# Optimization experiments

Measured on AMD Instinct MI355X. Metric: run time of the kernel, lower is better.

## Reference

```python
import jax, jax.numpy as jnp
import numpy as np

B, C, H, W = 16, 256, 96, 96
PLANES = 64            # inplanes * ratio = 256 * 0.25
HEADS = 4
EPS = 1e-5             # BatchNorm eps


def setup_inputs() -> dict:
    key = jax.random.key(0)
    ks = jax.random.split(key, 8)
    HW = H * W
    G = HW // HEADS    # group size of the grouped 1x1 conv over spatial-positions-as-channels
    return {
        "x": jax.random.normal(ks[0], (B, C, H, W), jnp.float32),
        # input_conv: Conv1x1(C->PLANES) -> BN -> ReLU -> Conv1x1(PLANES->C)
        "w1": jax.random.normal(ks[1], (PLANES, C), jnp.float32) * (1.0 / np.sqrt(C)),
        "b1": jax.random.normal(ks[2], (PLANES,), jnp.float32) * 0.01,
        "gamma": jnp.ones((PLANES,), jnp.float32),
        "beta": jnp.zeros((PLANES,), jnp.float32),
        "mean": jnp.zeros((PLANES,), jnp.float32),
        "var": jnp.ones((PLANES,), jnp.float32),
        "w2": jax.random.normal(ks[3], (C, PLANES), jnp.float32) * (1.0 / np.sqrt(PLANES)),
        "b2": jax.random.normal(ks[4], (C,), jnp.float32) * 0.01,
        # conv_mask: Conv2d(HW, HEADS, k=1, groups=HEADS) -> weight [HEADS, G], bias [HEADS]
        "wm": jax.random.normal(ks[5], (HEADS, G), jnp.float32) * (1.0 / np.sqrt(G)),
        "bm": jax.random.normal(ks[6], (HEADS,), jnp.float32) * 0.01,
    }


def reference(x, w1, b1, gamma, beta, mean, var, w2, b2, wm, bm):
    Bx, Cx, Hx, Wx = x.shape
    G = (Hx * Wx) // HEADS
    # ---- input_conv: 1x1 conv -> BN (inference) -> ReLU -> 1x1 conv ----
    h = jnp.einsum('bchw,pc->bphw', x, w1) + b1[None, :, None, None]
    scale = (gamma / jnp.sqrt(var + EPS))[None, :, None, None]
    h = jax.nn.relu((h - mean[None, :, None, None]) * scale + beta[None, :, None, None])
    y = jnp.einsum('bphw,cp->bchw', h, w2) + b2[None, :, None, None]
    # ---- treat spatial positions as channels: [B, HEADS, G, C] ----
    ix = y.transpose(0, 2, 3, 1).reshape(Bx, HEADS, G, Cx)
    # grouped 1x1 conv over HW-channels -> logits [B, HEADS, C]
    logits = jnp.einsum('bhgc,hg->bhc', ix, wm) + bm[None, :, None]
    # softmax over channel axis (torch dim=2 of [B, HEADS, C, 1])
    mask = jax.nn.softmax(logits, axis=2)
    # context pooling matmul: [B,HEADS,G,C] @ [B,HEADS,C,1] -> [B,HEADS,G]
    ctx = jnp.einsum('bhgc,bhc->bhg', ix, mask)
    context = ctx.reshape(Bx, 1, Hx, Wx)
    # fusion_types = ('channel_add',)
    return x + context
```

## Files before the change

kernel.cpp:

```cpp
#include <hip/hip_runtime.h>

#define Bn 16
#define Cn 256
#define HWn 9216
#define Pn 64
#define HEADSn 4
#define Gn 2304
#define STILE 64
#define TILES_PER_B (HWn / STILE)
#define NTILE (Bn * TILES_PER_B)
#define CHUNK 9
#define NBLK (NTILE / CHUNK)

typedef float f32x4 __attribute__((ext_vector_type(4)));
typedef short short4v __attribute__((ext_vector_type(4)));
typedef short short8 __attribute__((ext_vector_type(8)));

static __device__ __forceinline__ unsigned short f2bf(float f) {
    unsigned int b = __builtin_bit_cast(unsigned int, f);
    unsigned int r = b + 0x7FFFu + ((b >> 16) & 1u);
    return (unsigned short)(r >> 16);
}
static __device__ __forceinline__ float bf2f(unsigned short u) {
    unsigned int b = ((unsigned int)u) << 16;
    return __builtin_bit_cast(float, b);
}
static __device__ __forceinline__ void gload_lds16(const void* g, void* l) {
    __builtin_amdgcn_global_load_lds((const __attribute__((address_space(1))) void*)g,
                                     (__attribute__((address_space(3))) void*)l, 16, 0, 0);
}

__global__ __launch_bounds__(256)
void k0_prep(const float* __restrict__ w1, const float* __restrict__ b1,
             const float* __restrict__ gamma, const float* __restrict__ beta,
             const float* __restrict__ mean, const float* __restrict__ var,
             float* __restrict__ scbc, short* __restrict__ w1s)
{
    const int gid = blockIdx.x * 256 + threadIdx.x;
    if (gid < 2048) {
        const int row = gid >> 5;
        const int kc  = (gid & 31) << 3;
        const float* p = w1 + row * Cn + kc;
        short8 v;
        #pragma unroll
        for (int j = 0; j < 8; ++j) v[j] = (short)f2bf(p[j]);
        const int idx = (row * Cn + kc) ^ ((row & 7) << 3);
        *reinterpret_cast<short8*>(&w1s[idx]) = v;
    }
    if (gid < Pn) {
        float s = gamma[gid] * rsqrtf(var[gid] + 1e-5f);
        scbc[gid] = s;
        scbc[Pn + gid] = (b1[gid] - mean[gid]) * s + beta[gid];
    }
}

__global__ __launch_bounds__(256)
void k1_gemm(const float* __restrict__ x, const short* __restrict__ w1s,
             const float* __restrict__ scbc, const float* __restrict__ wm,
             float* __restrict__ hmp, short* __restrict__ hg)
{
    __shared__ short w1l[Pn * Cn];
    __shared__ short xl[2][Cn * STILE];
    __shared__ float hml[4][Pn];

    const int pid  = blockIdx.x;
    const int b    = pid / 16;
    const int t0b  = pid * CHUNK - b * TILES_PER_B;
    const int t    = threadIdx.x;
    const int lane = t & 63;
    const int wv   = t >> 6;
    const int g    = lane >> 4;
    const int m16  = lane & 15;
    const int sbase = wv * 16 + m16;

    #pragma unroll
    for (int i = 0; i < 8; ++i) {
        const int chunk = i * 4 + wv;
        gload_lds16(w1s + chunk * 512 + lane * 8, &w1l[chunk * 512]);
    }

    const int c0 = t >> 4;
    const int s4 = t & 15;
    const float* xbb = x + (size_t)b * Cn * HWn + s4 * 4;
    short* hgb = hg + (size_t)b * HWn * Pn;
    const float* scp = scbc;

    float sc[4][4], bc[4][4];
    #pragma unroll
    for (int rt = 0; rt < 4; ++rt)
        #pragma unroll
        for (int r = 0; r < 4; ++r) {
            const int p = rt * 16 + g * 4 + r;
            sc[rt][r] = scp[p];
            bc[rt][r] = scp[Pn + p];
        }

    float hmacc[4][4];
    #pragma unroll
    for (int rt = 0; rt < 4; ++rt)
        #pragma unroll
        for (int r = 0; r < 4; ++r) hmacc[rt][r] = 0.f;

    {
        const float* xb = xbb + (size_t)(t0b * STILE);
        f32x4 xa[16];
        #pragma unroll
        for (int i = 0; i < 16; ++i)
            xa[i] = *reinterpret_cast<const f32x4*>(xb + (size_t)(c0 + 16 * i) * HWn);
        #pragma unroll
        for (int i = 0; i < 16; ++i) {
            const int c = c0 + 16 * i;
            short4v v;
            #pragma unroll
            for (int j = 0; j < 4; ++j) v[j] = (short)f2bf(xa[i][j]);
            const int f   = (c & 7) ^ ((c >> 3) & 3);
            const int idx = (c * STILE + s4 * 4) ^ (f << 3);
            *reinterpret_cast<short4v*>(&xl[0][idx]) = v;
        }
    }
    __syncthreads();

    int cur = 0;
    for (int it = 0; it < CHUNK; ++it) {
        const int s0 = (t0b + it) * STILE;

        f32x4 xn[16];
        if (it < CHUNK - 1) {
            const float* xb = xbb + (size_t)(s0 + STILE);
            #pragma unroll
            for (int i = 0; i < 16; ++i)
                xn[i] = *reinterpret_cast<const f32x4*>(xb + (size_t)(c0 + 16 * i) * HWn);
        }

        const short* xc = xl[cur];
        f32x4 acc[4] = { {0,0,0,0}, {0,0,0,0}, {0,0,0,0}, {0,0,0,0} };
        #pragma unroll
        for (int ks = 0; ks < 8; ++ks) {
            short8 bf;
            #pragma unroll
            for (int j = 0; j < 8; ++j) {
                const int k = ks * 32 + g * 8 + j;
                bf[j] = xc[(k * STILE + sbase) ^ ((j ^ g) << 3)];
            }
            #pragma unroll
            for (int rt = 0; rt < 4; ++rt) {
                const int row = rt * 16 + m16;
                const int idx = (row * Cn + ks * 32 + g * 8) ^ ((row & 7) << 3);
                const short8 af = *reinterpret_cast<const short8*>(&w1l[idx]);
                acc[rt] = __builtin_amdgcn_mfma_f32_16x16x32_bf16(af, bf, acc[rt], 0, 0, 0);
            }
        }

        const float wmv = wm[s0 + sbase];
        short* hrow = hgb + (size_t)(s0 + sbase) * Pn;
        #pragma unroll
        for (int rt = 0; rt < 4; ++rt) {
            short4v hv;
            #pragma unroll
            for (int r = 0; r < 4; ++r) {
                float h = acc[rt][r] * sc[rt][r] + bc[rt][r];
                h = h > 0.f ? h : 0.f;
                hmacc[rt][r] = fmaf(h, wmv, hmacc[rt][r]);
                hv[r] = (short)f2bf(h);
            }
            *reinterpret_cast<short4v*>(hrow + rt * 16 + g * 4) = hv;
        }

        if (it < CHUNK - 1) {
            #pragma unroll
            for (int i = 0; i < 16; ++i) {
                const int c = c0 + 16 * i;
                short4v v;
                #pragma unroll
                for (int j = 0; j < 4; ++j) v[j] = (short)f2bf(xn[i][j]);
                const int f   = (c & 7) ^ ((c >> 3) & 3);
                const int idx = (c * STILE + s4 * 4) ^ (f << 3);
                *reinterpret_cast<short4v*>(&xl[cur ^ 1][idx]) = v;
            }
            __syncthreads();
            cur ^= 1;
        }
    }

    #pragma unroll
    for (int rt = 0; rt < 4; ++rt)
        #pragma unroll
        for (int r = 0; r < 4; ++r) {
            float v = hmacc[rt][r];
            v += __shfl_xor(v, 1); v += __shfl_xor(v, 2);
            v += __shfl_xor(v, 4); v += __shfl_xor(v, 8);
            hmacc[rt][r] = v;
        }
    if (m16 == 0) {
        #pragma unroll
        for (int rt = 0; rt < 4; ++rt) {
            f32x4 hv = { hmacc[rt][0], hmacc[rt][1], hmacc[rt][2], hmacc[rt][3] };
            *reinterpret_cast<f32x4*>(&hml[wv][rt * 16 + g * 4]) = hv;
        }
    }
    __syncthreads();
    if (t < Pn) hmp[pid * Pn + t] = hml[0][t] + hml[1][t] + hml[2][t] + hml[3][t];
}

__global__ __launch_bounds__(256)
void k2_mask(const float* __restrict__ hmp, const float* __restrict__ w2,
             const float* __restrict__ b2, const float* __restrict__ wm,
             float* __restrict__ wmix, float* __restrict__ bmix)
{
    __shared__ float hms[Pn];
    __shared__ float masks[Cn];
    __shared__ float red[4];
    __shared__ float part[4][Pn];

    const int bh = blockIdx.x;
    const int head = bh & (HEADSn - 1);
    const int t = threadIdx.x;
    const int l = t & 63;
    const int wv = t >> 6;

    {
        const int p = t & 63, q = t >> 6;
        part[q][p] = hmp[(bh * 4 + q) * Pn + p];
    }
    __syncthreads();
    if (t < Pn) hms[t] = part[0][t] + part[1][t] + part[2][t] + part[3][t];
    __syncthreads();

    float wsum = 0.f;
    for (int i = t; i < Gn; i += 256) wsum += wm[head * Gn + i];
    #pragma unroll
    for (int d = 1; d < 64; d <<= 1) wsum += __shfl_xor(wsum, d);
    if (l == 0) red[wv] = wsum;
    __syncthreads();
    wsum = red[0] + red[1] + red[2] + red[3];

    float lg = 0.f;
    #pragma unroll
    for (int k = 0; k < Pn; ++k) lg = fmaf(w2[t * Pn + k], hms[k], lg);
    lg = fmaf(b2[t], wsum, lg);

    float mx = lg;
    #pragma unroll
    for (int d = 1; d < 64; d <<= 1) mx = fmaxf(mx, __shfl_xor(mx, d));
    __syncthreads();
    if (l == 0) red[wv] = mx;
    __syncthreads();
    mx = fmaxf(fmaxf(red[0], red[1]), fmaxf(red[2], red[3]));
    const float ev = __expf(lg - mx);
    float sm = ev;
    #pragma unroll
    for (int d = 1; d < 64; d <<= 1) sm += __shfl_xor(sm, d);
    __syncthreads();
    if (l == 0) red[wv] = sm;
    __syncthreads();
    sm = red[0] + red[1] + red[2] + red[3];
    masks[t] = ev / sm;
    __syncthreads();

    {
        const int k = t & (Pn - 1);
        const int q = t >> 6;
        float wp = 0.f;
        #pragma unroll
        for (int i = 0; i < 64; ++i) {
            const int c = q * 64 + i;
            wp = fmaf(masks[c], w2[c * Pn + k], wp);
        }
        part[q][k] = wp;
    }
    __syncthreads();
    if (t < Pn) wmix[bh * Pn + t] = part[0][t] + part[1][t] + part[2][t] + part[3][t];

    float bp = masks[t] * b2[t];
    #pragma unroll
    for (int d = 1; d < 64; d <<= 1) bp += __shfl_xor(bp, d);
    __syncthreads();
    if (l == 0) red[wv] = bp;
    __syncthreads();
    if (t == 0) bmix[bh] = red[0] + red[1] + red[2] + red[3];
}

__global__ __launch_bounds__(256)
void k3_stream(const float* __restrict__ x, const short* __restrict__ hg,
               const float* __restrict__ wmix, const float* __restrict__ bmix,
               float* __restrict__ out)
{
    __shared__ float ctxl[STILE];

    const int bid  = blockIdx.x;
    const int b    = bid / TILES_PER_B;
    const int tile = bid % TILES_PER_B;
    const int s0   = tile * STILE;
    const int head = s0 / Gn;
    const int bh   = b * HEADSn + head;
    const int t    = threadIdx.x;

    if (t < STILE) {
        const short* hr = hg + ((size_t)b * HWn + s0 + t) * Pn;
        const float* wmx = wmix + bh * Pn;
        float acc = 0.f;
        #pragma unroll
        for (int i = 0; i < 8; ++i) {
            const short8 v = *reinterpret_cast<const short8*>(hr + i * 8);
            const f32x4 w0 = *reinterpret_cast<const f32x4*>(wmx + i * 8);
            const f32x4 w1v = *reinterpret_cast<const f32x4*>(wmx + i * 8 + 4);
            #pragma unroll
            for (int j = 0; j < 4; ++j) {
                acc = fmaf(bf2f((unsigned short)v[j]), w0[j], acc);
                acc = fmaf(bf2f((unsigned short)v[4 + j]), w1v[j], acc);
            }
        }
        ctxl[t] = acc + bmix[bh];
    }
    __syncthreads();

    const int c0 = t >> 4;
    const int s4 = t & 15;
    const f32x4 cv = *reinterpret_cast<const f32x4*>(&ctxl[s4 * 4]);
    const float* xb = x + (size_t)b * Cn * HWn + s0 + s4 * 4;
    float* ob = out + (size_t)b * Cn * HWn + s0 + s4 * 4;
    #pragma unroll
    for (int i = 0; i < 16; ++i) {
        const size_t off = (size_t)(c0 + 16 * i) * HWn;
        *reinterpret_cast<f32x4*>(ob + off) =
            *reinterpret_cast<const f32x4*>(xb + off) + cv;
    }
}

extern "C" void kernel_launch(void* const* d_in, const int* in_sizes, int n_in,
                              void* d_out, int out_size, void* d_ws, size_t ws_size,
                              hipStream_t stream)
{
    (void)in_sizes; (void)n_in; (void)out_size; (void)ws_size;
    const float* x     = (const float*)d_in[0];
    const float* w1    = (const float*)d_in[1];
    const float* b1    = (const float*)d_in[2];
    const float* gamma = (const float*)d_in[3];
    const float* beta  = (const float*)d_in[4];
    const float* mean  = (const float*)d_in[5];
    const float* var   = (const float*)d_in[6];
    const float* w2    = (const float*)d_in[7];
    const float* b2    = (const float*)d_in[8];
    const float* wm    = (const float*)d_in[9];

    float* out  = (float*)d_out;
    float* wsf  = (float*)d_ws;
    float* hmp  = wsf;
    float* wmix = hmp + NBLK * Pn;
    float* bmix = wmix + Bn * HEADSn * Pn;
    float* scbc = bmix + 64;
    short* w1s  = (short*)(scbc + 128);
    short* hg   = w1s + Pn * Cn;

    k0_prep<<<dim3(8), dim3(256), 0, stream>>>(w1, b1, gamma, beta, mean, var, scbc, w1s);
    k1_gemm<<<dim3(NBLK), dim3(256), 0, stream>>>(x, w1s, scbc, wm, hmp, hg);
    k2_mask<<<dim3(Bn * HEADSn), dim3(256), 0, stream>>>(hmp, w2, b2, wm, wmix, bmix);
    k3_stream<<<dim3(NTILE / 1), dim3(256), 0, stream>>>(x, hg, wmix, bmix, out);
}
```

Before: 101.6 us.

## Stream x tiles into LDS asynchronously as fp32, keep W1 in registers

The first GEMM kernel now copies fp32 x tiles straight from global memory into LDS with direct global-to-LDS loads, issued one tile ahead. This replaces the old path that loaded into registers, converted to bf16 and stored to LDS, and it converts to bf16 when LDS is read. The BN scale is folded into W1 in the prep kernel, and each wave holds its whole W1 fragment in registers instead of LDS. The intent is to cut register staging and let loads overlap the MFMA work. The costs are double the LDS footprint (fp32 tiles, 128KB, hence launch_bounds(256,1)), more LDS read traffic, conversion work in the inner loop, and heavy register pressure from the 32 short8 W1 fragments.

```diff
diff --git a/kernel.cpp b/kernel.cpp
--- a/kernel.cpp
+++ b/kernel.cpp
@@ -34,66 +34,56 @@
 void k0_prep(const float* __restrict__ w1, const float* __restrict__ b1,
              const float* __restrict__ gamma, const float* __restrict__ beta,
              const float* __restrict__ mean, const float* __restrict__ var,
-             float* __restrict__ scbc, short* __restrict__ w1s)
+             float* __restrict__ bcv, short* __restrict__ w1b)
 {
     const int gid = blockIdx.x * 256 + threadIdx.x;
     if (gid < 2048) {
         const int row = gid >> 5;
-        const int kc  = (gid & 31) << 3;
-        const float* p = w1 + row * Cn + kc;
+        const float s = gamma[row] * rsqrtf(var[row] + 1e-5f);
+        const float* p = w1 + gid * 8;
         short8 v;
         #pragma unroll
-        for (int j = 0; j < 8; ++j) v[j] = (short)f2bf(p[j]);
-        const int idx = (row * Cn + kc) ^ ((row & 7) << 3);
-        *reinterpret_cast<short8*>(&w1s[idx]) = v;
+        for (int j = 0; j < 8; ++j) v[j] = (short)f2bf(p[j] * s);
+        *reinterpret_cast<short8*>(&w1b[gid * 8]) = v;
     }
     if (gid < Pn) {
-        float s = gamma[gid] * rsqrtf(var[gid] + 1e-5f);
-        scbc[gid] = s;
-        scbc[Pn + gid] = (b1[gid] - mean[gid]) * s + beta[gid];
-    }
-}
-
-__global__ __launch_bounds__(256)
-void k1_gemm(const float* __restrict__ x, const short* __restrict__ w1s,
-             const float* __restrict__ scbc, const float* __restrict__ wm,
+        const float s = gamma[gid] * rsqrtf(var[gid] + 1e-5f);
+        bcv[gid] = (b1[gid] - mean[gid]) * s + beta[gid];
+    }
+}
+
+__global__ __launch_bounds__(256, 1)
+void k1_gemm(const float* __restrict__ x, const short* __restrict__ w1b,
+             const float* __restrict__ bcv, const float* __restrict__ wm,
              float* __restrict__ hmp, short* __restrict__ hg)
 {
-    __shared__ short w1l[Pn * Cn];
-    __shared__ short xl[2][Cn * STILE];
+    __shared__ float xl[2][Cn * STILE];
     __shared__ float hml[4][Pn];
 
     const int pid  = blockIdx.x;
-    const int b    = pid / 16;
-    const int t0b  = pid * CHUNK - b * TILES_PER_B;
+    const int b    = pid >> 4;
+    const int t0b  = (pid & 15) * CHUNK;
     const int t    = threadIdx.x;
     const int lane = t & 63;
     const int wv   = t >> 6;
+    const int wvu  = __builtin_amdgcn_readfirstlane(wv);
     const int g    = lane >> 4;
     const int m16  = lane & 15;
     const int sbase = wv * 16 + m16;
 
-    #pragma unroll
-    for (int i = 0; i < 8; ++i) {
-        const int chunk = i * 4 + wv;
-        gload_lds16(w1s + chunk * 512 + lane * 8, &w1l[chunk * 512]);
-    }
-
-    const int c0 = t >> 4;
-    const int s4 = t & 15;
-    const float* xbb = x + (size_t)b * Cn * HWn + s4 * 4;
-    short* hgb = hg + (size_t)b * HWn * Pn;
-    const float* scp = scbc;
-
-    float sc[4][4], bc[4][4];
+    short8 af[4][8];
     #pragma unroll
     for (int rt = 0; rt < 4; ++rt)
         #pragma unroll
-        for (int r = 0; r < 4; ++r) {
-            const int p = rt * 16 + g * 4 + r;
-            sc[rt][r] = scp[p];
-            bc[rt][r] = scp[Pn + p];
-        }
+        for (int ks = 0; ks < 8; ++ks)
+            af[rt][ks] = *reinterpret_cast<const short8*>(
+                w1b + (rt * 16 + m16) * Cn + ks * 32 + g * 8);
+
+    float bc[4][4];
+    #pragma unroll
+    for (int rt = 0; rt < 4; ++rt)
+        #pragma unroll
+        for (int r = 0; r < 4; ++r) bc[rt][r] = bcv[rt * 16 + g * 4 + r];
 
     float hmacc[4][4];
     #pragma unroll
@@ -101,38 +91,33 @@
         #pragma unroll
         for (int r = 0; r < 4; ++r) hmacc[rt][r] = 0.f;
 
-    {
-        const float* xb = xbb + (size_t)(t0b * STILE);
-        f32x4 xa[16];
-        #pragma unroll
-        for (int i = 0; i < 16; ++i)
-            xa[i] = *reinterpret_cast<const f32x4*>(xb + (size_t)(c0 + 16 * i) * HWn);
-        #pragma unroll
-        for (int i = 0; i < 16; ++i) {
-            const int c = c0 + 16 * i;
-            short4v v;
-            #pragma unroll
-            for (int j = 0; j < 4; ++j) v[j] = (short)f2bf(xa[i][j]);
-            const int f   = (c & 7) ^ ((c >> 3) & 3);
-            const int idx = (c * STILE + s4 * 4) ^ (f << 3);
-            *reinterpret_cast<short4v*>(&xl[0][idx]) = v;
-        }
-    }
+    const float* xbb = x + (size_t)b * Cn * HWn;
+
+    #define STAGE(buf, tile)                                                     \
+        do {                                                                     \
+            const int _s0 = (tile) * STILE;                                      \
+            _Pragma("unroll")                                                    \
+            for (int i = 0; i < 16; ++i) {                                       \
+                const int cbase = wvu * 64 + i * 4;                              \
+                const int c     = cbase + g;                                     \
+                const int gc    = (c >> 3) & 3;                                  \
+                const int soff  = (m16 * 4) ^ (gc << 4);                         \
+                gload_lds16(xbb + (size_t)c * HWn + _s0 + soff,                  \
+                            &xl[buf][cbase * 64]);                               \
+            }                                                                    \
+        } while (0)
+
+    STAGE(0, t0b);
     __syncthreads();
 
     int cur = 0;
     for (int it = 0; it < CHUNK; ++it) {
+        if (it + 1 < CHUNK) STAGE(cur ^ 1, t0b + it + 1);
+
         const int s0 = (t0b + it) * STILE;
-
-        f32x4 xn[16];
-        if (it < CHUNK - 1) {
-            const float* xb = xbb + (size_t)(s0 + STILE);
-            #pragma unroll
-            for (int i = 0; i < 16; ++i)
-                xn[i] = *reinterpret_cast<const f32x4*>(xb + (size_t)(c0 + 16 * i) * HWn);
-        }
-
-        const short* xc = xl[cur];
+        const float* xc = xl[cur];
+        const int srd = sbase ^ (g << 4);
+
         f32x4 acc[4] = { {0,0,0,0}, {0,0,0,0}, {0,0,0,0}, {0,0,0,0} };
         #pragma unroll
         for (int ks = 0; ks < 8; ++ks) {
@@ -140,25 +125,21 @@
             #pragma unroll
             for (int j = 0; j < 8; ++j) {
                 const int k = ks * 32 + g * 8 + j;
-                bf[j] = xc[(k * STILE + sbase) ^ ((j ^ g) << 3)];
+                bf[j] = (short)f2bf(xc[k * 64 + srd]);
             }
             #pragma unroll
-            for (int rt = 0; rt < 4; ++rt) {
-                const int row = rt * 16 + m16;
-                const int idx = (row * Cn + ks * 32 + g * 8) ^ ((row & 7) << 3);
-                const short8 af = *reinterpret_cast<const short8*>(&w1l[idx]);
-                acc[rt] = __builtin_amdgcn_mfma_f32_16x16x32_bf16(af, bf, acc[rt], 0, 0, 0);
-            }
+            for (int rt = 0; rt < 4; ++rt)
+                acc[rt] = __builtin_amdgcn_mfma_f32_16x16x32_bf16(af[rt][ks], bf, acc[rt], 0, 0, 0);
         }
 
         const float wmv = wm[s0 + sbase];
-        short* hrow = hgb + (size_t)(s0 + sbase) * Pn;
+        short* hrow = hg + ((size_t)b * HWn + s0 + sbase) * Pn;
         #pragma unroll
         for (int rt = 0; rt < 4; ++rt) {
             short4v hv;
             #pragma unroll
             for (int r = 0; r < 4; ++r) {
-                float h = acc[rt][r] * sc[rt][r] + bc[rt][r];
+                float h = acc[rt][r] + bc[rt][r];
                 h = h > 0.f ? h : 0.f;
                 hmacc[rt][r] = fmaf(h, wmv, hmacc[rt][r]);
                 hv[r] = (short)f2bf(h);
@@ -166,20 +147,8 @@
             *reinterpret_cast<short4v*>(hrow + rt * 16 + g * 4) = hv;
         }
 
-        if (it < CHUNK - 1) {
-            #pragma unroll
-            for (int i = 0; i < 16; ++i) {
-                const int c = c0 + 16 * i;
-                short4v v;
-                #pragma unroll
-                for (int j = 0; j < 4; ++j) v[j] = (short)f2bf(xn[i][j]);
-                const int f   = (c & 7) ^ ((c >> 3) & 3);
-                const int idx = (c * STILE + s4 * 4) ^ (f << 3);
-                *reinterpret_cast<short4v*>(&xl[cur ^ 1][idx]) = v;
-            }
-            __syncthreads();
-            cur ^= 1;
-        }
+        __syncthreads();
+        cur ^= 1;
     }
 
     #pragma unroll
@@ -348,12 +317,12 @@
     float* hmp  = wsf;
     float* wmix = hmp + NBLK * Pn;
     float* bmix = wmix + Bn * HEADSn * Pn;
-    float* scbc = bmix + 64;
-    short* w1s  = (short*)(scbc + 128);
-    short* hg   = w1s + Pn * Cn;
-
-    k0_prep<<<dim3(8), dim3(256), 0, stream>>>(w1, b1, gamma, beta, mean, var, scbc, w1s);
-    k1_gemm<<<dim3(NBLK), dim3(256), 0, stream>>>(x, w1s, scbc, wm, hmp, hg);
+    float* bcv  = bmix + 64;
+    short* w1b  = (short*)(bcv + 64);
+    short* hg   = w1b + Pn * Cn;
+
+    k0_prep<<<dim3(8), dim3(256), 0, stream>>>(w1, b1, gamma, beta, mean, var, bcv, w1b);
+    k1_gemm<<<dim3(NBLK), dim3(256), 0, stream>>>(x, w1b, bcv, wm, hmp, hg);
     k2_mask<<<dim3(Bn * HEADSn), dim3(256), 0, stream>>>(hmp, w2, b2, wm, wmix, bmix);
-    k3_stream<<<dim3(NTILE / 1), dim3(256), 0, stream>>>(x, hg, wmix, bmix, out);
-}
+    k3_stream<<<dim3(NTILE), dim3(256), 0, stream>>>(x, hg, wmix, bmix, out);
+}
```

Measured after the change: 107.8 us. +6.1%, slower.
